# Kernel optimization log

Measured on AMD Instinct MI355X. Metric: run time of the kernel, lower is better.

## Reference

```python
import jax, jax.numpy as jnp
import numpy as np

N_NODES = 100000
N_EDGES = 1600000
D_IN = 256
D_OUT = 128


def setup_inputs() -> dict:
    key = jax.random.key(0)
    k1, k2, k3, k4, k5, k6 = jax.random.split(key, 6)
    inp = {
        "input": jax.random.normal(k1, (N_NODES, D_IN), dtype=jnp.float32),
        "edge_row": jax.random.randint(k2, (N_EDGES,), 0, N_NODES),
        "edge_col": jax.random.randint(k3, (N_EDGES,), 0, N_NODES),
        "edge_val": jax.random.uniform(k4, (N_EDGES,), dtype=jnp.float32),
        "W": jax.random.normal(k5, (D_IN, D_OUT), dtype=jnp.float32) * (1.0 / np.sqrt(D_IN)),
        "b": jax.random.normal(k6, (D_OUT,), dtype=jnp.float32) * 0.01,
    }
    return inp


def reference(input, edge_row, edge_col, edge_val, W, b):
    # support = Linear(input)  -> [N, D_OUT]
    support = jnp.dot(input, W) + b
    # sparse.mm(adj, support): out[r] = sum_e val[e] * support[col[e]] for edges with row[e]==r
    msgs = edge_val[:, None] * support[edge_col]  # [E, D_OUT]
    agg = jax.ops.segment_sum(msgs, edge_row, num_segments=N_NODES)  # [N, D_OUT]
    return jnp.tanh(agg)
```

## Files before the change

kernel.cpp:

```cpp
#include <hip/hip_runtime.h>
#include <math.h>

#define N_NODES 100000
#define N_EDGES 1600000
#define D_IN 256
#define D_OUT 128

#define OFF_SUPPORT 0
#define OFF_COUNTS  51200000
#define OFF_CSREV   51600008
#define OFF_BSUMS   64400008
#define OFF_WTHI    64400416
#define OFF_WTLO    64465952

#define SCAN_CHUNK  1024
#define SCAN_BLOCKS ((N_NODES + SCAN_CHUNK - 1) / SCAN_CHUNK)

#define GB 128
#define GEMM_BLOCKS ((N_NODES + GB - 1) / GB)
#define EDGE_BLOCKS ((N_EDGES + 255) / 256)

typedef __attribute__((ext_vector_type(8))) short s8v;
typedef __attribute__((ext_vector_type(4))) float f4v;

__device__ __forceinline__ short f2bf(float x) {
  unsigned u = __float_as_uint(x);
  unsigned r = u + 0x7FFF + ((u >> 16) & 1);
  return (short)(r >> 16);
}
__device__ __forceinline__ float bf2f(short h) {
  return __uint_as_float(((unsigned)(unsigned short)h) << 16);
}

__device__ __forceinline__ void cvt8(float4 a, float4 b, s8v& h, s8v& l) {
  float f[8] = {a.x, a.y, a.z, a.w, b.x, b.y, b.z, b.w};
#pragma unroll
  for (int i = 0; i < 8; i++) {
    short hh = f2bf(f[i]);
    h[i] = hh;
    l[i] = f2bf(f[i] - bf2f(hh));
  }
}

__device__ __forceinline__ void gload_lds16(const void* g, void* l) {
  __builtin_amdgcn_global_load_lds(
      (const __attribute__((address_space(1))) void*)g,
      (__attribute__((address_space(3))) void*)l, 16, 0, 0);
}

#define VMW(N)                                             \
  asm volatile("s_waitcnt vmcnt(" #N ")" ::: "memory");    \
  __builtin_amdgcn_sched_barrier(0)
#define SBAR()                    \
  __builtin_amdgcn_s_barrier();   \
  __builtin_amdgcn_sched_barrier(0)

__global__ __launch_bounds__(256) void wconv_kernel(
    const float* __restrict__ W, short* __restrict__ wt_hi,
    short* __restrict__ wt_lo, int* __restrict__ counts) {
  int idx = blockIdx.x * 256 + threadIdx.x;
  int k = idx >> 7;
  int n = idx & 127;
  float v = W[idx];
  short h = f2bf(v);
  wt_hi[n * 256 + k] = h;
  wt_lo[n * 256 + k] = f2bf(v - bf2f(h));
  for (int i = idx; i < N_NODES + 1; i += 32768) counts[i] = 0;
}

__device__ __forceinline__ void gemm_body(
    int gb, const float* __restrict__ input, const short* __restrict__ wt_hi,
    const short* __restrict__ wt_lo, const float* __restrict__ b,
    float* __restrict__ support) {
  __shared__ short Bh[2][128][64];
  __shared__ short Bl[2][128][64];
  const int t = threadIdx.x;
  const int lane = t & 63;
  const int wv = t >> 6;
  const int qm = lane & 15;
  const int quad = lane >> 4;
  const int node0 = gb * GB;

  int r0 = node0 + wv * 32 + qm;
  int r1 = r0 + 16;
  if (r0 > N_NODES - 1) r0 = N_NODES - 1;
  if (r1 > N_NODES - 1) r1 = N_NODES - 1;
  const float* a0p = input + (size_t)r0 * D_IN + quad * 8;
  const float* a1p = input + (size_t)r1 * D_IN + quad * 8;

  const int lrow = lane >> 3;
  const int lpc = lane & 7;
  auto stageB = [&](int q, int p) {
    const int rb = wv * 32;
#pragma unroll
    for (int j = 0; j < 4; ++j) {
      int n = rb + j * 8 + lrow;
      int sc = lpc ^ (n & 7);
      const short* sh = wt_hi + (size_t)n * 256 + q * 64 + sc * 8;
      const short* sl = wt_lo + (size_t)n * 256 + q * 64 + sc * 8;
      gload_lds16(sh, &Bh[p][rb + j * 8][0]);
      gload_lds16(sl, &Bl[p][rb + j * 8][0]);
    }
  };

  float4 A0[4], A1[4], A2[4];
  auto loadA = [&](float4* d, int s) {
    d[0] = *(const float4*)(a0p + s * 32);
    d[1] = *(const float4*)(a0p + s * 32 + 4);
    d[2] = *(const float4*)(a1p + s * 32);
    d[3] = *(const float4*)(a1p + s * 32 + 4);
  };

  f4v acc[2][8];
#pragma unroll
  for (int mt = 0; mt < 2; mt++)
#pragma unroll
    for (int nt = 0; nt < 8; nt++) acc[mt][nt] = (f4v){0.f, 0.f, 0.f, 0.f};

  s8v ah0, al0, ah1, al1;
  auto cvtA = [&](const float4* X) {
    cvt8(X[0], X[1], ah0, al0);
    cvt8(X[2], X[3], ah1, al1);
  };
  auto mfma8 = [&](int p, int si) {
#pragma unroll
    for (int nt = 0; nt < 8; ++nt) {
      int n = nt * 16 + qm;
      int pc = (si * 4 + quad) ^ (n & 7);
      s8v bh = *(const s8v*)&Bh[p][n][pc * 8];
      s8v bl = *(const s8v*)&Bl[p][n][pc * 8];
      acc[0][nt] = __builtin_amdgcn_mfma_f32_16x16x32_bf16(ah0, bh, acc[0][nt], 0, 0, 0);
      acc[0][nt] = __builtin_amdgcn_mfma_f32_16x16x32_bf16(ah0, bl, acc[0][nt], 0, 0, 0);
      acc[0][nt] = __builtin_amdgcn_mfma_f32_16x16x32_bf16(al0, bh, acc[0][nt], 0, 0, 0);
      acc[1][nt] = __builtin_amdgcn_mfma_f32_16x16x32_bf16(ah1, bh, acc[1][nt], 0, 0, 0);
      acc[1][nt] = __builtin_amdgcn_mfma_f32_16x16x32_bf16(ah1, bl, acc[1][nt], 0, 0, 0);
      acc[1][nt] = __builtin_amdgcn_mfma_f32_16x16x32_bf16(al1, bh, acc[1][nt], 0, 0, 0);
    }
  };

  stageB(0, 0);
  loadA(A0, 0);
  loadA(A1, 1);
  loadA(A2, 2);
  VMW(8);
  SBAR();
  cvtA(A0);
  stageB(1, 1);
  loadA(A0, 3);
  mfma8(0, 0);
  VMW(16);
  cvtA(A1);
  loadA(A1, 4);
  mfma8(0, 1);
  VMW(8);
  SBAR();
  cvtA(A2);
  stageB(2, 0);
  loadA(A2, 5);
  mfma8(1, 0);
  VMW(16);
  cvtA(A0);
  loadA(A0, 6);
  mfma8(1, 1);
  VMW(8);
  SBAR();
  cvtA(A1);
  stageB(3, 1);
  loadA(A1, 7);
  mfma8(0, 0);
  VMW(16);
  cvtA(A2);
  mfma8(0, 1);
  VMW(4);
  SBAR();
  cvtA(A0);
  mfma8(1, 0);
  VMW(0);
  cvtA(A1);
  mfma8(1, 1);

  float bias[8];
#pragma unroll
  for (int nt = 0; nt < 8; nt++) bias[nt] = b[nt * 16 + qm];
#pragma unroll
  for (int mt = 0; mt < 2; mt++) {
#pragma unroll
    for (int nt = 0; nt < 8; nt++) {
      int col = nt * 16 + qm;
#pragma unroll
      for (int r = 0; r < 4; r++) {
        int node = node0 + wv * 32 + mt * 16 + quad * 4 + r;
        if (node < N_NODES)
          support[(size_t)node * D_OUT + col] = acc[mt][nt][r] + bias[nt];
      }
    }
  }
}

__global__ __launch_bounds__(256, 2) void gemm_hist_kernel(
    const float* __restrict__ input, const short* __restrict__ wt_hi,
    const short* __restrict__ wt_lo, const float* __restrict__ b,
    float* __restrict__ support, const int* __restrict__ erow,
    int* __restrict__ counts, int* __restrict__ pos_e) {
  if (blockIdx.x < GEMM_BLOCKS) {
    gemm_body(blockIdx.x, input, wt_hi, wt_lo, b, support);
  } else {
    int e = (blockIdx.x - GEMM_BLOCKS) * 256 + threadIdx.x;
    if (e < N_EDGES) pos_e[e] = atomicAdd(&counts[erow[e]], 1);
  }
}

__global__ __launch_bounds__(256) void build_kernel(
    const int* __restrict__ erow, const int* __restrict__ ecol,
    const float* __restrict__ eval, const int* __restrict__ offsets,
    const int* __restrict__ pos_e, long long* __restrict__ csr_ev) {
  int e = blockIdx.x * 256 + threadIdx.x;
  if (e < N_EDGES) {
    int r = __builtin_nontemporal_load(erow + e);
    int c = __builtin_nontemporal_load(ecol + e);
    int vb = __builtin_nontemporal_load((const int*)eval + e);
    int p = __builtin_nontemporal_load(pos_e + e);
    int idx = offsets[r] + p;
    long long packed = (unsigned int)c | ((long long)(unsigned int)vb << 32);
    __builtin_nontemporal_store(packed, csr_ev + idx);
  }
}

__global__ __launch_bounds__(256) void scan_phase1(const int* __restrict__ counts,
                                                   int* __restrict__ bsums) {
  __shared__ int ts[256];
  int t = threadIdx.x;
  int idx0 = blockIdx.x * SCAN_CHUNK + t * 4;
  int s = 0;
#pragma unroll
  for (int i = 0; i < 4; i++)
    if (idx0 + i < N_NODES) s += counts[idx0 + i];
  ts[t] = s;
  __syncthreads();
#pragma unroll
  for (int off = 128; off > 0; off >>= 1) {
    if (t < off) ts[t] += ts[t + off];
    __syncthreads();
  }
  if (t == 0) bsums[blockIdx.x] = ts[0];
}

__global__ __launch_bounds__(128) void scan_phase2(int* __restrict__ bsums) {
  __shared__ int s[128];
  int t = threadIdx.x;
  int v = (t < SCAN_BLOCKS) ? bsums[t] : 0;
  s[t] = v;
  __syncthreads();
#pragma unroll
  for (int off = 1; off < 128; off <<= 1) {
    int x = (t >= off) ? s[t - off] : 0;
    __syncthreads();
    s[t] += x;
    __syncthreads();
  }
  if (t < SCAN_BLOCKS) bsums[t] = s[t] - v;
}

__global__ __launch_bounds__(256) void scan_phase3(int* __restrict__ counts,
                                                   const int* __restrict__ bsums) {
  __shared__ int ts[256];
  int t = threadIdx.x;
  int b = blockIdx.x;
  int idx0 = b * SCAN_CHUNK + t * 4;
  int v[4];
  int s = 0;
#pragma unroll
  for (int i = 0; i < 4; i++) {
    v[i] = (idx0 + i < N_NODES) ? counts[idx0 + i] : 0;
    s += v[i];
  }
  ts[t] = s;
  __syncthreads();
#pragma unroll
  for (int off = 1; off < 256; off <<= 1) {
    int x = (t >= off) ? ts[t - off] : 0;
    __syncthreads();
    ts[t] += x;
    __syncthreads();
  }
  int run = bsums[b] + ts[t] - s;
#pragma unroll
  for (int i = 0; i < 4; i++) {
    int idx = idx0 + i;
    if (idx < N_NODES) counts[idx] = run;
    run += v[i];
  }
  if (b == 0 && t == 0) counts[N_NODES] = N_EDGES;
}

__global__ __launch_bounds__(256) void agg_kernel(
    const int* __restrict__ offsets, const long long* __restrict__ csr_ev,
    const float* __restrict__ support, float* __restrict__ out) {
  int r = blockIdx.x * 8 + (threadIdx.x >> 5);
  int l4 = (threadIdx.x & 31) * 4;
  int beg = offsets[r];
  int end = offsets[r + 1];
  float4 acc = make_float4(0.f, 0.f, 0.f, 0.f);

  if (end > beg) {
    int ec[8], encol[8];
    float ev[8], env[8];
#pragma unroll
    for (int u = 0; u < 8; u++) {
      int idx = beg + u;
      int c = idx < end ? idx : end - 1;
      long long p = __builtin_nontemporal_load(csr_ev + c);
      ec[u] = (int)(unsigned int)p;
      ev[u] = (idx < end) ? __uint_as_float((unsigned int)(p >> 32)) : 0.f;
    }
    for (int j = beg; j < end; j += 8) {
      int jn = j + 8;
      if (jn < end) {
#pragma unroll
        for (int u = 0; u < 8; u++) {
          int idx = jn + u;
          int c = idx < end ? idx : end - 1;
          long long p = __builtin_nontemporal_load(csr_ev + c);
          encol[u] = (int)(unsigned int)p;
          env[u] = (idx < end) ? __uint_as_float((unsigned int)(p >> 32)) : 0.f;
        }
      }
      float4 s[8];
#pragma unroll
      for (int u = 0; u < 8; u++)
        s[u] = *(const float4*)(support + (size_t)ec[u] * D_OUT + l4);
#pragma unroll
      for (int u = 0; u < 8; u++) {
        acc.x = fmaf(ev[u], s[u].x, acc.x);
        acc.y = fmaf(ev[u], s[u].y, acc.y);
        acc.z = fmaf(ev[u], s[u].z, acc.z);
        acc.w = fmaf(ev[u], s[u].w, acc.w);
      }
#pragma unroll
      for (int u = 0; u < 8; u++) { ec[u] = encol[u]; ev[u] = env[u]; }
    }
  }
  *(float4*)(out + (size_t)r * D_OUT + l4) =
      make_float4(tanhf(acc.x), tanhf(acc.y), tanhf(acc.z), tanhf(acc.w));
}

extern "C" void kernel_launch(void* const* d_in, const int* in_sizes, int n_in,
                              void* d_out, int out_size, void* d_ws, size_t ws_size,
                              hipStream_t stream) {
  const float* input = (const float*)d_in[0];
  const int* erow = (const int*)d_in[1];
  const int* ecol = (const int*)d_in[2];
  const float* eval = (const float*)d_in[3];
  const float* W = (const float*)d_in[4];
  const float* b = (const float*)d_in[5];
  float* out = (float*)d_out;

  char* ws = (char*)d_ws;
  float* support = (float*)(ws + OFF_SUPPORT);
  int* counts = (int*)(ws + OFF_COUNTS);
  long long* csr_ev = (long long*)(ws + OFF_CSREV);
  int* bsums = (int*)(ws + OFF_BSUMS);
  short* wt_hi = (short*)(ws + OFF_WTHI);
  short* wt_lo = (short*)(ws + OFF_WTLO);
  int* pos_e = (int*)d_out;

  hipLaunchKernelGGL(wconv_kernel, dim3((D_IN * D_OUT) / 256), dim3(256), 0,
                     stream, W, wt_hi, wt_lo, counts);
  hipLaunchKernelGGL(gemm_hist_kernel, dim3(GEMM_BLOCKS + EDGE_BLOCKS),
                     dim3(256), 0, stream, input, wt_hi, wt_lo, b, support,
                     erow, counts, pos_e);
  hipLaunchKernelGGL(scan_phase1, dim3(SCAN_BLOCKS), dim3(256), 0, stream,
                     counts, bsums);
  hipLaunchKernelGGL(scan_phase2, dim3(1), dim3(128), 0, stream, bsums);
  hipLaunchKernelGGL(scan_phase3, dim3(SCAN_BLOCKS), dim3(256), 0, stream,
                     counts, bsums);
  hipLaunchKernelGGL(build_kernel, dim3(EDGE_BLOCKS), dim3(256), 0, stream,
                     erow, ecol, eval, counts, pos_e, csr_ev);
  hipLaunchKernelGGL(agg_kernel, dim3(N_NODES / 8), dim3(256), 0, stream,
                     counts, csr_ev, support, out);
}
```

Baseline: 422.4 us.

## Overlap GEMM with CSR build instead of histogram; move histogram into prep

The edge-row histogram moves from the GEMM launch into the weight-conversion launch, and the CSR build kernel is fused with the GEMM so the build's scattered writes share a launch with the compute-bound GEMM blocks. Counts are now zeroed with a memset, and the nontemporal hints on the CSR store and the aggregation loads become ordinary accesses so the packed edges can stay in cache for the aggregation pass. This changes which memory-bound phase runs alongside the GEMM. The histogram atomics now run in a small launch with no overlap, and the memset adds one more launch.

Result: no change. 422.7 us (+0.1%).

```diff
diff --git a/kernel.cpp b/kernel.cpp
--- a/kernel.cpp
+++ b/kernel.cpp
@@ -19,6 +19,7 @@
 #define GB 128
 #define GEMM_BLOCKS ((N_NODES + GB - 1) / GB)
 #define EDGE_BLOCKS ((N_EDGES + 255) / 256)
+#define WCONV_BLOCKS ((D_IN * D_OUT) / 256)
 
 typedef __attribute__((ext_vector_type(8))) short s8v;
 typedef __attribute__((ext_vector_type(4))) float f4v;
@@ -55,17 +56,22 @@
   __builtin_amdgcn_s_barrier();   \
   __builtin_amdgcn_sched_barrier(0)
 
-__global__ __launch_bounds__(256) void wconv_kernel(
+__global__ __launch_bounds__(256) void prep_kernel(
     const float* __restrict__ W, short* __restrict__ wt_hi,
-    short* __restrict__ wt_lo, int* __restrict__ counts) {
-  int idx = blockIdx.x * 256 + threadIdx.x;
-  int k = idx >> 7;
-  int n = idx & 127;
-  float v = W[idx];
-  short h = f2bf(v);
-  wt_hi[n * 256 + k] = h;
-  wt_lo[n * 256 + k] = f2bf(v - bf2f(h));
-  for (int i = idx; i < N_NODES + 1; i += 32768) counts[i] = 0;
+    short* __restrict__ wt_lo, const int* __restrict__ erow,
+    int* __restrict__ counts, int* __restrict__ pos_e) {
+  if (blockIdx.x < WCONV_BLOCKS) {
+    int idx = blockIdx.x * 256 + threadIdx.x;
+    int k = idx >> 7;
+    int n = idx & 127;
+    float v = W[idx];
+    short h = f2bf(v);
+    wt_hi[n * 256 + k] = h;
+    wt_lo[n * 256 + k] = f2bf(v - bf2f(h));
+  } else {
+    int e = (blockIdx.x - WCONV_BLOCKS) * 256 + threadIdx.x;
+    if (e < N_EDGES) pos_e[e] = atomicAdd(&counts[erow[e]], 1);
+  }
 }
 
 __device__ __forceinline__ void gemm_body(
@@ -197,32 +203,26 @@
   }
 }
 
-__global__ __launch_bounds__(256, 2) void gemm_hist_kernel(
+__global__ __launch_bounds__(256, 2) void gemm_build_kernel(
     const float* __restrict__ input, const short* __restrict__ wt_hi,
     const short* __restrict__ wt_lo, const float* __restrict__ b,
     float* __restrict__ support, const int* __restrict__ erow,
-    int* __restrict__ counts, int* __restrict__ pos_e) {
+    const int* __restrict__ ecol, const float* __restrict__ eval,
+    const int* __restrict__ offsets, const int* __restrict__ pos_e,
+    long long* __restrict__ csr_ev) {
   if (blockIdx.x < GEMM_BLOCKS) {
     gemm_body(blockIdx.x, input, wt_hi, wt_lo, b, support);
   } else {
     int e = (blockIdx.x - GEMM_BLOCKS) * 256 + threadIdx.x;
-    if (e < N_EDGES) pos_e[e] = atomicAdd(&counts[erow[e]], 1);
-  }
-}
-
-__global__ __launch_bounds__(256) void build_kernel(
-    const int* __restrict__ erow, const int* __restrict__ ecol,
-    const float* __restrict__ eval, const int* __restrict__ offsets,
-    const int* __restrict__ pos_e, long long* __restrict__ csr_ev) {
-  int e = blockIdx.x * 256 + threadIdx.x;
-  if (e < N_EDGES) {
-    int r = __builtin_nontemporal_load(erow + e);
-    int c = __builtin_nontemporal_load(ecol + e);
-    int vb = __builtin_nontemporal_load((const int*)eval + e);
-    int p = __builtin_nontemporal_load(pos_e + e);
-    int idx = offsets[r] + p;
-    long long packed = (unsigned int)c | ((long long)(unsigned int)vb << 32);
-    __builtin_nontemporal_store(packed, csr_ev + idx);
+    if (e < N_EDGES) {
+      int r = __builtin_nontemporal_load(erow + e);
+      int c = __builtin_nontemporal_load(ecol + e);
+      int vb = __builtin_nontemporal_load((const int*)eval + e);
+      int p = __builtin_nontemporal_load(pos_e + e);
+      int idx = offsets[r] + p;
+      long long packed = (unsigned int)c | ((long long)(unsigned int)vb << 32);
+      csr_ev[idx] = packed;
+    }
   }
 }
 
@@ -309,7 +309,7 @@
     for (int u = 0; u < 8; u++) {
       int idx = beg + u;
       int c = idx < end ? idx : end - 1;
-      long long p = __builtin_nontemporal_load(csr_ev + c);
+      long long p = csr_ev[c];
       ec[u] = (int)(unsigned int)p;
       ev[u] = (idx < end) ? __uint_as_float((unsigned int)(p >> 32)) : 0.f;
     }
@@ -320,7 +320,7 @@
         for (int u = 0; u < 8; u++) {
           int idx = jn + u;
           int c = idx < end ? idx : end - 1;
-          long long p = __builtin_nontemporal_load(csr_ev + c);
+          long long p = csr_ev[c];
           encol[u] = (int)(unsigned int)p;
           env[u] = (idx < end) ? __uint_as_float((unsigned int)(p >> 32)) : 0.f;
         }
@@ -364,17 +364,17 @@
   short* wt_lo = (short*)(ws + OFF_WTLO);
   int* pos_e = (int*)d_out;
 
-  hipLaunchKernelGGL(wconv_kernel, dim3((D_IN * D_OUT) / 256), dim3(256), 0,
-                     stream, W, wt_hi, wt_lo, counts);
-  hipLaunchKernelGGL(gemm_hist_kernel, dim3(GEMM_BLOCKS + EDGE_BLOCKS),
-                     dim3(256), 0, stream, input, wt_hi, wt_lo, b, support,
-                     erow, counts, pos_e);
+  hipMemsetAsync(ws + OFF_COUNTS, 0, (size_t)(N_NODES + 1) * 4, stream);
+
+  hipLaunchKernelGGL(prep_kernel, dim3(WCONV_BLOCKS + EDGE_BLOCKS), dim3(256),
+                     0, stream, W, wt_hi, wt_lo, erow, counts, pos_e);
   hipLaunchKernelGGL(scan_phase1, dim3(SCAN_BLOCKS), dim3(256), 0, stream,
                      counts, bsums);
   hipLaunchKernelGGL(scan_phase2, dim3(1), dim3(128), 0, stream, bsums);
   hipLaunchKernelGGL(scan_phase3, dim3(SCAN_BLOCKS), dim3(256), 0, stream,
                      counts, bsums);
-  hipLaunchKernelGGL(build_kernel, dim3(EDGE_BLOCKS), dim3(256), 0, stream,
+  hipLaunchKernelGGL(gemm_build_kernel, dim3(GEMM_BLOCKS + EDGE_BLOCKS),
+                     dim3(256), 0, stream, input, wt_hi, wt_lo, b, support,
                      erow, ecol, eval, counts, pos_e, csr_ev);
   hipLaunchKernelGGL(agg_kernel, dim3(N_NODES / 8), dim3(256), 0, stream,
                      counts, csr_ev, support, out);
```
